# Optimization experiments

Measured on AMD Instinct MI355X. Metric: run time of the kernel, lower is better.

Reference implementation:

```python
import jax, jax.numpy as jnp
import numpy as np

N = 200_000      # nodes
E = 6_400_000    # edges (avg degree 32)
G = 2_000        # graphs
SD = 10          # state_dim
ROUNDS = 3


def setup_inputs() -> dict:
    key = jax.random.key(0)
    ks = jax.random.split(key, 10)
    node_coordinates = jax.random.normal(ks[0], (N, 3), dtype=jnp.float32)
    node_graph_index = jnp.sort(jax.random.randint(ks[1], (N,), 0, G))
    node_from = jax.random.randint(ks[2], (E,), 0, N)
    node_to = jax.random.randint(ks[3], (E,), 0, N)
    edge_lengths = jax.random.uniform(ks[4], (E, 1), dtype=jnp.float32)
    edge_vectors = jax.random.normal(ks[5], (E, 3), dtype=jnp.float32)
    # message net: Linear(14 -> 10), torch default uniform init
    lim = 1.0 / np.sqrt(SD + 4)
    W_msg = jax.random.uniform(ks[6], (SD + 4, SD), minval=-lim, maxval=lim, dtype=jnp.float32)
    b_msg = jax.random.uniform(ks[7], (SD,), minval=-lim, maxval=lim, dtype=jnp.float32)
    # output net: Linear(10 -> 4), xavier_normal weight, default bias
    W_out = jax.random.normal(ks[8], (SD, 4), dtype=jnp.float32) * np.float32(np.sqrt(2.0 / (SD + 4)))
    lim_o = 1.0 / np.sqrt(SD)
    b_out = jax.random.uniform(ks[9], (4,), minval=-lim_o, maxval=lim_o, dtype=jnp.float32)
    return dict(node_coordinates=node_coordinates, edge_lengths=edge_lengths,
                edge_vectors=edge_vectors, W_msg=W_msg, b_msg=b_msg,
                W_out=W_out, b_out=b_out, node_from=node_from, node_to=node_to,
                node_graph_index=node_graph_index, num_nodes=N, num_graphs=G)


def reference(node_coordinates, edge_lengths, edge_vectors, W_msg, b_msg,
              W_out, b_out, node_from, node_to, node_graph_index,
              num_nodes, num_graphs):
    c_from = node_coordinates[node_from]                      # (E,3) gather
    c_to = node_coordinates[node_to]                          # (E,3) gather
    coord_sum = jnp.sum(jnp.abs(c_from), axis=1, keepdims=True)       # (E,1)
    dot1 = jnp.sum(c_from * c_to, axis=1, keepdims=True)              # (E,1)
    dot2 = jnp.sum(c_from * edge_vectors, axis=1, keepdims=True)      # (E,1)
    geo = jnp.concatenate([edge_lengths, coord_sum, dot1, dot2], axis=1)  # (E,4), identical every round

    state = jnp.zeros((num_nodes, SD), dtype=node_coordinates.dtype)
    for _ in range(ROUNDS):
        inp = jnp.concatenate([state[node_from], geo], axis=1)        # (E,14)
        msg = jnp.tanh(inp @ W_msg + b_msg)                           # (E,10)
        state = state + jax.ops.segment_sum(msg, node_to, num_segments=num_nodes)

    graph_state = jax.ops.segment_sum(state, node_graph_index, num_segments=num_graphs)  # (G,10)
    ev = graph_state @ W_out + b_out                                  # (G,4)
    gamma, v, alpha, beta = jnp.split(ev, 4, axis=1)
    sp = jax.nn.softplus
    return jnp.concatenate([gamma, sp(v), sp(alpha) + 1.0, sp(beta)], axis=1)
```

## Files before the change

### kernel.cpp

```cpp
#include <hip/hip_runtime.h>
#include <hip/hip_fp16.h>
#include <math.h>

#define SD 10
#define BSZ 64
#define EB 512
#define CTHR 1024
#define BINB 10
#define NBIN_MAX 256

typedef unsigned uvec4 __attribute__((ext_vector_type(4)));
struct rec12 { unsigned x, y, z; };
union U32H2 { unsigned u; __half2 h; };

__device__ __forceinline__ float tanh_fast(float x) {
    float e = __expf(2.0f * x);
    float r = __builtin_amdgcn_rcpf(1.0f + e);
    return 1.0f - 2.0f * r;
}

__device__ __forceinline__ float softplus_f(float x) {
    return fmaxf(x, 0.0f) + log1pf(expf(-fabsf(x)));
}


__global__ __launch_bounds__(256) void coords4_kernel(
    const float* __restrict__ coords, float4* __restrict__ coords4, int N)
{
    int n = blockIdx.x * blockDim.x + threadIdx.x;
    if (n >= N) return;
    float4 c;
    c.x = coords[n * 3 + 0];
    c.y = coords[n * 3 + 1];
    c.z = coords[n * 3 + 2];
    c.w = 0.0f;
    coords4[n] = c;
}


__global__ __launch_bounds__(CTHR) void pass1_kernel(
    const float4* __restrict__ coords4,
    const float* __restrict__ elen,
    const float* __restrict__ evec,
    const int* __restrict__ nfrom,
    const int* __restrict__ nto,
    unsigned* __restrict__ s1addr,
    uvec4* __restrict__ payA,
    int E, int NBIN)
{
    __shared__ unsigned hbin[NBIN_MAX];
    __shared__ unsigned curbin[NBIN_MAX];
    int b = blockIdx.x, t = threadIdx.x;
    long long ebeg = (long long)E * b / EB;
    long long eend = (long long)E * (b + 1) / EB;

    if (t < NBIN_MAX) hbin[t] = 0;
    __syncthreads();
    for (long long e = ebeg + t; e < eend; e += CTHR)
        atomicAdd(&hbin[((unsigned)nto[e]) >> BINB], 1u);
    __syncthreads();
    {
        unsigned v = (t < NBIN_MAX) ? hbin[t] : 0u;
        for (int d = 1; d < NBIN_MAX; d <<= 1) {
            unsigned x = (t < NBIN_MAX && t >= d) ? hbin[t - d] : 0u;
            __syncthreads();
            if (t < NBIN_MAX) hbin[t] += x;
            __syncthreads();
        }
        if (t < NBIN_MAX) curbin[t] = (unsigned)ebeg + hbin[t] - v;
    }
    __syncthreads();
    if (t < NBIN) s1addr[(size_t)t * EB + b] = curbin[t];
    if (t == 0)  s1addr[(size_t)NBIN * EB + b] = (unsigned)eend;
    __syncthreads();

    long long e = ebeg + t;
    if (e < eend) {
        int nf0 = nfrom[e], nt0 = nto[e];
        float4 cf0 = coords4[nf0];
        float l0 = elen[e];
        float ex0 = evec[e*3+0], ey0 = evec[e*3+1], ez0 = evec[e*3+2];
        while (true) {
            long long e1 = e + CTHR;
            bool has1 = e1 < eend;
            int nf1 = 0, nt1 = 0; float4 cf1 = cf0;
            float l1 = 0, ex1 = 0, ey1 = 0, ez1 = 0;
            if (has1) {
                nf1 = nfrom[e1]; nt1 = nto[e1];
                cf1 = coords4[nf1];
                l1 = elen[e1]; ex1 = evec[e1*3+0]; ey1 = evec[e1*3+1]; ez1 = evec[e1*3+2];
            }
            unsigned bin = ((unsigned)nt0) >> BINB;
            unsigned pos = atomicAdd(&curbin[bin], 1u);
            float g1 = fabsf(cf0.x) + fabsf(cf0.y) + fabsf(cf0.z);
            float g3 = cf0.x * ex0 + cf0.y * ey0 + cf0.z * ez0;
            U32H2 a, c, d;
            a.h = __floats2half2_rn(l0, g1);
            c.h = __floats2half2_rn(g3, cf0.x);
            d.h = __floats2half2_rn(cf0.y, cf0.z);
            uvec4 p;
            p.x = (unsigned)nf0 | (((unsigned)nt0 & ((1u << BINB) - 1u)) << 18);
            p.y = a.u; p.z = c.u; p.w = d.u;
            payA[pos] = p;
            if (!has1) break;
            e = e1; nf0 = nf1; nt0 = nt1; cf0 = cf1;
            l0 = l1; ex0 = ex1; ey0 = ey1; ez0 = ez1;
        }
    }
}

__global__ __launch_bounds__(256) void colsum_kernel(
    const unsigned* __restrict__ s1addr, unsigned* __restrict__ binsum)
{
    __shared__ unsigned red[256];
    int q = blockIdx.x, t = threadIdx.x;
    red[t] = s1addr[(size_t)q * EB + t] + s1addr[(size_t)q * EB + t + 256];
    __syncthreads();
    for (int d = 128; d > 0; d >>= 1) {
        if (t < d) red[t] += red[t + d];
        __syncthreads();
    }
    if (t == 0) binsum[q] = red[0];
}

__global__ __launch_bounds__(256) void binstart_kernel(
    const unsigned* __restrict__ binsum, unsigned* __restrict__ binstart,
    unsigned* __restrict__ nodestart, int NBIN, int E)
{
    int t = threadIdx.x;
    unsigned b0 = binsum[0];
    for (int q = t; q <= NBIN; q += 256) binstart[q] = binsum[q] - b0;
    if (t == 0) nodestart[(size_t)NBIN << BINB] = (unsigned)E;
}

__global__ __launch_bounds__(CTHR) void pass2_kernel(
    const unsigned* __restrict__ s1addr,
    const unsigned* __restrict__ binstart,
    const float4* __restrict__ coords4,
    const uvec4* __restrict__ src,
    rec12* __restrict__ dst,
    unsigned* __restrict__ nodestart,
    int NBIN)
{
    __shared__ unsigned segst[EB];
    __shared__ unsigned spref[EB + 1];
    __shared__ unsigned hist[1 << BINB];
    __shared__ unsigned cur[1 << BINB];
    int q = blockIdx.x, t = threadIdx.x;

    if (t < EB) {
        unsigned st = s1addr[(size_t)q * EB + t];
        unsigned en = s1addr[(size_t)(q + 1) * EB + t];
        segst[t] = st;
        spref[t] = en - st;
    }
    hist[t] = 0;
    __syncthreads();
    {
        unsigned v = (t < EB) ? spref[t] : 0u;
        for (int d = 1; d < EB; d <<= 1) {
            unsigned x = (t < EB && t >= d) ? spref[t - d] : 0u;
            __syncthreads();
            if (t < EB) spref[t] += x;
            __syncthreads();
        }
        unsigned incl = (t < EB) ? spref[t] : 0u;
        __syncthreads();
        if (t < EB) spref[t] = incl - v;
        if (t == EB - 1) spref[EB] = incl;
    }
    __syncthreads();
    unsigned len = spref[EB];
    unsigned obase = binstart[q];
    const unsigned* srcw = (const unsigned*)src;

    for (unsigned i = t; i < len; i += CTHR) {
        unsigned lo = 0, hi = EB;
#pragma unroll
        for (int s = 0; s < 9; s++) {
            unsigned mid = (lo + hi) >> 1;
            if (spref[mid] <= i) lo = mid; else hi = mid;
        }
        unsigned x0 = srcw[(size_t)(segst[lo] + (i - spref[lo])) * 4];
        atomicAdd(&hist[(x0 >> 18) & ((1u << BINB) - 1u)], 1u);
    }
    __syncthreads();
    unsigned hv = hist[t];
    __syncthreads();
    for (int d = 1; d < (1 << BINB); d <<= 1) {
        unsigned x = (t >= d) ? hist[t - d] : 0u;
        __syncthreads();
        hist[t] += x;
        __syncthreads();
    }
    unsigned excl = hist[t] - hv;
    cur[t] = obase + excl;
    nodestart[((size_t)q << BINB) + t] = obase + excl;
    __syncthreads();

    for (unsigned i = t; i < len; i += CTHR) {
        unsigned lo = 0, hi = EB;
#pragma unroll
        for (int s = 0; s < 9; s++) {
            unsigned mid = (lo + hi) >> 1;
            if (spref[mid] <= i) lo = mid; else hi = mid;
        }
        uvec4 p = src[segst[lo] + (i - spref[lo])];
        unsigned key = (p.x >> 18) & ((1u << BINB) - 1u);
        unsigned pos = atomicAdd(&cur[key], 1u);
        unsigned nt = ((unsigned)q << BINB) | key;
        float4 ct = coords4[nt];
        U32H2 zc, wc;
        zc.u = p.z; wc.u = p.w;
        float g3 = __low2float(zc.h);
        float cfx = __high2float(zc.h);
        float cfy = __low2float(wc.h), cfz = __high2float(wc.h);
        float g2 = cfx * ct.x + cfy * ct.y + cfz * ct.z;
        U32H2 o; o.h = __floats2half2_rn(g2, g3);
        rec12 r;
        r.x = (p.x & 0x3FFFFu) | ((nt & (BSZ - 1u)) << 18);
        r.y = p.y;
        r.z = o.u;
        dst[pos] = r;
    }
}


__global__ __launch_bounds__(256) void wstate_kernel(
    const float* __restrict__ state, const float* __restrict__ Wm,
    const float* __restrict__ bm, __half* __restrict__ wsth, int N)
{
    int n = blockIdx.x * blockDim.x + threadIdx.x;
    if (n >= N) return;
    const float2* sp = (const float2*)(state + (size_t)n * SD);
    float s[SD];
#pragma unroll
    for (int h = 0; h < 5; h++) { float2 v = sp[h]; s[2*h] = v.x; s[2*h+1] = v.y; }
    float t[SD];
#pragma unroll
    for (int j = 0; j < SD; j++) t[j] = bm[j];
#pragma unroll
    for (int k = 0; k < SD; k++) {
#pragma unroll
        for (int j = 0; j < SD; j++) t[j] += s[k] * Wm[k * SD + j];
    }
    unsigned* dp = (unsigned*)(wsth + (size_t)n * SD);
#pragma unroll
    for (int h = 0; h < 5; h++) {
        U32H2 cv;
        cv.h = __floats2half2_rn(t[2*h], t[2*h+1]);
        dp[h] = cv.u;
    }
}

template <bool FIRST>
__global__ __launch_bounds__(256) void round_run_kernel(
    const unsigned* __restrict__ nodestart,
    const rec12* __restrict__ payload,
    const float* __restrict__ Wm,
    const float* __restrict__ bm,
    const __half* __restrict__ wsth,
    const float* __restrict__ state_prev,
    float* __restrict__ state_next,
    int N, int E)
{
    __shared__ float acc[BSZ * SD];
    int k = blockIdx.x;
    for (int i = threadIdx.x; i < BSZ * SD; i += 256) acc[i] = 0.0f;

    int lane = threadIdx.x & 63;
    int wv = threadIdx.x >> 6;
    int grp0 = lane / 10;
    bool active = grp0 < 6;
    int grp = active ? grp0 : 5;
    int j = active ? (lane - grp0 * 10) : (lane - 60);

    float w0 = Wm[10 * SD + j];
    float w1 = Wm[11 * SD + j];
    float w2 = Wm[12 * SD + j];
    float w3 = Wm[13 * SD + j];
    float bb = bm[j];
    __syncthreads();

    unsigned beg = nodestart[(size_t)k << 6];
    unsigned end = nodestart[(size_t)(k + 1) << 6];
    unsigned len = end - beg;
    unsigned Q = (len + 3) >> 2;
    unsigned rbeg = beg + (unsigned)wv * Q;
    unsigned rend = rbeg + Q; if (rend > end) rend = end;
    unsigned eclamp = (unsigned)E - 1u;

    unsigned e0 = rbeg + (unsigned)grp;
    rec12 P0 = payload[e0 <= eclamp ? e0 : eclamp];
    unsigned e1 = e0 + 6;
    rec12 P1 = payload[e1 <= eclamp ? e1 : eclamp];
    float T0 = bb, T1 = bb;
    if (!FIRST) T0 = __half2float(wsth[(size_t)(P0.x & 0x3FFFFu) * SD + j]);

    int cur_lnt = -1;
    float accv = 0.0f;

    for (unsigned base = rbeg; base < rend; base += 6) {
        unsigned e2 = base + 12 + (unsigned)grp;
        rec12 P2 = payload[e2 <= eclamp ? e2 : eclamp];
        if (!FIRST) T1 = __half2float(wsth[(size_t)(P1.x & 0x3FFFFu) * SD + j]);
        unsigned e = base + (unsigned)grp;
        if (active && e < rend) {
            int lnt = (int)((P0.x >> 18) & (BSZ - 1));
            U32H2 c01, c23;
            c01.u = P0.y; c23.u = P0.z;
            float g0 = __low2float(c01.h), g1 = __high2float(c01.h);
            float g2 = __low2float(c23.h), g3 = __high2float(c23.h);
            float t = T0 + g0 * w0 + g1 * w1 + g2 * w2 + g3 * w3;
            if (lnt != cur_lnt) {
                if (cur_lnt >= 0) atomicAdd(&acc[cur_lnt * SD + j], accv);
                accv = 0.0f;
                cur_lnt = lnt;
            }
            accv += tanh_fast(t);
        }
        P0 = P1; P1 = P2; T0 = T1;
    }
    if (active && cur_lnt >= 0) atomicAdd(&acc[cur_lnt * SD + j], accv);
    __syncthreads();

    int base_o = k * BSZ * SD;
    int lim = N * SD - base_o;
    for (int i = threadIdx.x; i < BSZ * SD; i += 256) {
        if (i < lim) {
            float v = acc[i];
            if (!FIRST) v += state_prev[base_o + i];
            state_next[base_o + i] = v;
        }
    }
}


__global__ __launch_bounds__(256) void goff_kernel(
    const int* __restrict__ gidx, unsigned* __restrict__ goff, int N, int G)
{
    int n = blockIdx.x * blockDim.x + threadIdx.x;
    if (n >= N) return;
    int g = gidx[n];
    if (n == 0) {
        for (int q = 0; q <= g; q++) goff[q] = 0;
    } else {
        int gp = gidx[n - 1];
        for (int q = gp + 1; q <= g; q++) goff[q] = (unsigned)n;
    }
    if (n == N - 1) {
        for (int q = g + 1; q <= G; q++) goff[q] = (unsigned)N;
    }
}

__global__ __launch_bounds__(256) void gsum_kernel(
    const float* __restrict__ state, const unsigned* __restrict__ goff,
    float* __restrict__ gstate, int G)
{
    int tid = blockIdx.x * blockDim.x + threadIdx.x;
    if (tid >= G * SD * 4) return;
    int s = tid & 3;
    int rest = tid >> 2;
    int g = rest / SD;
    int j = rest - g * SD;
    unsigned beg = goff[g], end = goff[g + 1];
    unsigned len = end - beg;
    unsigned b0 = beg + (len * (unsigned)s) / 4u;
    unsigned b1 = beg + (len * (unsigned)(s + 1)) / 4u;
    float a = 0.0f;
    for (unsigned n = b0; n < b1; n++) a += state[(size_t)n * SD + j];
    atomicAdd(&gstate[(size_t)g * SD + j], a);
}

__global__ __launch_bounds__(256) void out_kernel(
    const float* __restrict__ gstate, const float* __restrict__ Wo,
    const float* __restrict__ bo, float* __restrict__ out, int G)
{
    int g = blockIdx.x * blockDim.x + threadIdx.x;
    if (g >= G) return;
    float s[SD];
#pragma unroll
    for (int k = 0; k < SD; k++) s[k] = gstate[(size_t)g * SD + k];
    float ev[4];
#pragma unroll
    for (int c = 0; c < 4; c++) {
        float a = bo[c];
#pragma unroll
        for (int k = 0; k < SD; k++) a += s[k] * Wo[k * 4 + c];
        ev[c] = a;
    }
    out[g * 4 + 0] = ev[0];
    out[g * 4 + 1] = softplus_f(ev[1]);
    out[g * 4 + 2] = softplus_f(ev[2]) + 1.0f;
    out[g * 4 + 3] = softplus_f(ev[3]);
}


template <bool FIRST>
__global__ __launch_bounds__(256) void edge_kernel_fb(
    const float* __restrict__ coords, const float* __restrict__ elen,
    const float* __restrict__ evec, const float* __restrict__ Wm,
    const float* __restrict__ bm, const int* __restrict__ nfrom,
    const int* __restrict__ nto, const float* __restrict__ state_prev,
    float* __restrict__ state_next, int E)
{
    int e = blockIdx.x * blockDim.x + threadIdx.x;
    if (e >= E) return;
    int nf = nfrom[e];
    int nt = nto[e];
    float cf0 = coords[nf*3+0], cf1 = coords[nf*3+1], cf2 = coords[nf*3+2];
    float ct0 = coords[nt*3+0], ct1 = coords[nt*3+1], ct2 = coords[nt*3+2];
    float ev0 = evec[e*3+0], ev1 = evec[e*3+1], ev2 = evec[e*3+2];
    float g0 = elen[e];
    float g1 = fabsf(cf0) + fabsf(cf1) + fabsf(cf2);
    float g2 = cf0*ct0 + cf1*ct1 + cf2*ct2;
    float g3 = cf0*ev0 + cf1*ev1 + cf2*ev2;
    float acc[SD];
#pragma unroll
    for (int j = 0; j < SD; j++) {
        acc[j] = bm[j] + g0*Wm[10*SD+j] + g1*Wm[11*SD+j] + g2*Wm[12*SD+j] + g3*Wm[13*SD+j];
    }
    if (!FIRST) {
        const float2* sp = (const float2*)(state_prev + (size_t)nf * SD);
        float s[SD];
#pragma unroll
        for (int h = 0; h < 5; h++) { float2 v = sp[h]; s[2*h] = v.x; s[2*h+1] = v.y; }
#pragma unroll
        for (int k = 0; k < SD; k++) {
#pragma unroll
            for (int j = 0; j < SD; j++) acc[j] += s[k] * Wm[k*SD+j];
        }
    }
    float* dst = state_next + (size_t)nt * SD;
#pragma unroll
    for (int j = 0; j < SD; j++) atomicAdd(dst + j, tanh_fast(acc[j]));
}

__global__ __launch_bounds__(256) void graph_reduce_fb(
    const float* __restrict__ state, const int* __restrict__ gidx,
    float* __restrict__ gstate, int N)
{
    int n = blockIdx.x * blockDim.x + threadIdx.x;
    if (n >= N) return;
    int g = gidx[n];
    const float2* sp = (const float2*)(state + (size_t)n * SD);
    float* dst = gstate + (size_t)g * SD;
#pragma unroll
    for (int h = 0; h < 5; h++) {
        float2 v = sp[h];
        atomicAdd(dst + 2*h, v.x);
        atomicAdd(dst + 2*h + 1, v.y);
    }
}


extern "C" void kernel_launch(void* const* d_in, const int* in_sizes, int n_in,
                              void* d_out, int out_size, void* d_ws, size_t ws_size,
                              hipStream_t stream) {
    const float* coords = (const float*)d_in[0];
    const float* elen   = (const float*)d_in[1];
    const float* evec   = (const float*)d_in[2];
    const float* Wm     = (const float*)d_in[3];
    const float* bm     = (const float*)d_in[4];
    const float* Wo     = (const float*)d_in[5];
    const float* bo     = (const float*)d_in[6];
    const int* nfrom    = (const int*)d_in[7];
    const int* nto      = (const int*)d_in[8];
    const int* gidx     = (const int*)d_in[9];

    const int E = in_sizes[1];
    const int N = in_sizes[9];
    const int G = out_size / 4;

    const int NBIN = (N + (1 << BINB) - 1) >> BINB;
    const int NB   = (N + BSZ - 1) / BSZ;

    const int BLK = 256;
    const int ng = (N + BLK - 1) / BLK;
    const int gg = (G + BLK - 1) / BLK;

    auto align256 = [](size_t x) { return (x + 255) & ~(size_t)255; };
    const size_t state_bytes = align256((size_t)N * SD * sizeof(float));
    const size_t wst_bytes   = align256((size_t)N * SD * sizeof(__half) + 256);
    const size_t payA_bytes  = align256((size_t)E * sizeof(uvec4));
    const size_t payB_bytes  = align256((size_t)E * sizeof(rec12) + 256);
    const size_t s1a_bytes   = align256((size_t)(NBIN_MAX + 1) * EB * sizeof(unsigned));
    const size_t bsum_bytes  = align256((size_t)(NBIN_MAX + 1) * sizeof(unsigned));
    const size_t nst_bytes   = align256(((size_t)NBIN_MAX * (1 << BINB) + 2) * sizeof(unsigned));
    const size_t goff_bytes  = align256((size_t)(G + 1) * sizeof(unsigned));
    const size_t gst_bytes   = align256((size_t)G * SD * sizeof(float));
    const size_t c4_bytes    = align256((size_t)N * sizeof(float4));

    size_t o = 0;
    char* w = (char*)d_ws;
    float* stateA      = (float*)(w + o);    o += state_bytes;
    float* stateB      = (float*)(w + o);    o += state_bytes;
    __half* wsth       = (__half*)(w + o);   o += wst_bytes;
    uvec4* payA        = (uvec4*)(w + o);    o += payA_bytes;
    rec12* payB        = (rec12*)(w + o);    o += payB_bytes;
    unsigned* s1addr   = (unsigned*)(w + o); o += s1a_bytes;
    unsigned* binsum   = (unsigned*)(w + o); o += bsum_bytes;
    unsigned* binstart = (unsigned*)(w + o); o += bsum_bytes;
    unsigned* nodestart= (unsigned*)(w + o); o += nst_bytes;
    unsigned* goff     = (unsigned*)(w + o); o += goff_bytes;
    float* gstate      = (float*)(w + o);    o += gst_bytes;
    float4* coords4    = (float4*)(w + o);   o += c4_bytes;

    if (o <= ws_size && NBIN <= NBIN_MAX && N < (1 << 18)) {
        coords4_kernel<<<ng, BLK, 0, stream>>>(coords, coords4, N);
        pass1_kernel<<<EB, CTHR, 0, stream>>>(coords4, elen, evec, nfrom, nto,
                                              s1addr, payA, E, NBIN);
        colsum_kernel<<<NBIN + 1, 256, 0, stream>>>(s1addr, binsum);
        binstart_kernel<<<1, 256, 0, stream>>>(binsum, binstart, nodestart, NBIN, E);
        pass2_kernel<<<NBIN, CTHR, 0, stream>>>(s1addr, binstart, coords4,
                                                payA, payB, nodestart, NBIN);
        round_run_kernel<true><<<NB, BLK, 0, stream>>>(nodestart, payB, Wm, bm,
                                                       wsth, stateB, stateA, N, E);
        wstate_kernel<<<ng, BLK, 0, stream>>>(stateA, Wm, bm, wsth, N);
        round_run_kernel<false><<<NB, BLK, 0, stream>>>(nodestart, payB, Wm, bm,
                                                        wsth, stateA, stateB, N, E);
        wstate_kernel<<<ng, BLK, 0, stream>>>(stateB, Wm, bm, wsth, N);
        round_run_kernel<false><<<NB, BLK, 0, stream>>>(nodestart, payB, Wm, bm,
                                                        wsth, stateB, stateA, N, E);
        hipMemsetAsync(gstate, 0, (size_t)G * SD * sizeof(float), stream);
        goff_kernel<<<ng, BLK, 0, stream>>>(gidx, goff, N, G);
        gsum_kernel<<<(G * SD * 4 + BLK - 1) / BLK, BLK, 0, stream>>>(stateA, goff, gstate, G);
        out_kernel<<<gg, BLK, 0, stream>>>(gstate, Wo, bo, (float*)d_out, G);
    } else {
        const int eg = (E + BLK - 1) / BLK;
        float* gstateF = (float*)(w + 2 * state_bytes);
        hipMemsetAsync(stateA, 0, state_bytes, stream);
        hipMemsetAsync(gstateF, 0, (size_t)G * SD * sizeof(float), stream);
        edge_kernel_fb<true><<<eg, BLK, 0, stream>>>(coords, elen, evec, Wm, bm,
                                                     nfrom, nto, stateA, stateA, E);
        hipMemcpyAsync(stateB, stateA, state_bytes, hipMemcpyDeviceToDevice, stream);
        edge_kernel_fb<false><<<eg, BLK, 0, stream>>>(coords, elen, evec, Wm, bm,
                                                      nfrom, nto, stateA, stateB, E);
        hipMemcpyAsync(stateA, stateB, state_bytes, hipMemcpyDeviceToDevice, stream);
        edge_kernel_fb<false><<<eg, BLK, 0, stream>>>(coords, elen, evec, Wm, bm,
                                                      nfrom, nto, stateB, stateA, E);
        graph_reduce_fb<<<ng, BLK, 0, stream>>>(stateA, gidx, gstateF, N);
        out_kernel<<<gg, BLK, 0, stream>>>(gstateF, Wo, bo, (float*)d_out, G);
    }
}
```

Before: 726.0 us.

## Move source-coordinate gather from pass1 to pass2 and shrink payload records

The first binning pass no longer gathers source coordinates. It writes a 12-byte record holding the edge length and edge vector in half precision, down from 16 bytes, and its streaming input loads are marked nontemporal. The second pass now gathers the source coordinates (with the abs-sum precomputed in coords4.w), computes both dot products, and software-pipelines the next record and coordinate load. This cuts intermediate payload traffic and moves the random gather to a pass with better locality. The cost is an extra gather in pass2 and the edge vector stored in half precision before the dot product, which changes rounding.

```diff
diff --git a/kernel.cpp b/kernel.cpp
--- a/kernel.cpp
+++ b/kernel.cpp
@@ -33,19 +33,18 @@
     c.x = coords[n * 3 + 0];
     c.y = coords[n * 3 + 1];
     c.z = coords[n * 3 + 2];
-    c.w = 0.0f;
+    c.w = fabsf(c.x) + fabsf(c.y) + fabsf(c.z);
     coords4[n] = c;
 }
 
 
 __global__ __launch_bounds__(CTHR) void pass1_kernel(
-    const float4* __restrict__ coords4,
     const float* __restrict__ elen,
     const float* __restrict__ evec,
     const int* __restrict__ nfrom,
     const int* __restrict__ nto,
     unsigned* __restrict__ s1addr,
-    uvec4* __restrict__ payA,
+    rec12* __restrict__ payA,
     int E, int NBIN)
 {
     __shared__ unsigned hbin[NBIN_MAX];
@@ -57,7 +56,7 @@
     if (t < NBIN_MAX) hbin[t] = 0;
     __syncthreads();
     for (long long e = ebeg + t; e < eend; e += CTHR)
-        atomicAdd(&hbin[((unsigned)nto[e]) >> BINB], 1u);
+        atomicAdd(&hbin[((unsigned)__builtin_nontemporal_load(&nto[e])) >> BINB], 1u);
     __syncthreads();
     {
         unsigned v = (t < NBIN_MAX) ? hbin[t] : 0u;
@@ -74,38 +73,23 @@
     if (t == 0)  s1addr[(size_t)NBIN * EB + b] = (unsigned)eend;
     __syncthreads();
 
-    long long e = ebeg + t;
-    if (e < eend) {
-        int nf0 = nfrom[e], nt0 = nto[e];
-        float4 cf0 = coords4[nf0];
-        float l0 = elen[e];
-        float ex0 = evec[e*3+0], ey0 = evec[e*3+1], ez0 = evec[e*3+2];
-        while (true) {
-            long long e1 = e + CTHR;
-            bool has1 = e1 < eend;
-            int nf1 = 0, nt1 = 0; float4 cf1 = cf0;
-            float l1 = 0, ex1 = 0, ey1 = 0, ez1 = 0;
-            if (has1) {
-                nf1 = nfrom[e1]; nt1 = nto[e1];
-                cf1 = coords4[nf1];
-                l1 = elen[e1]; ex1 = evec[e1*3+0]; ey1 = evec[e1*3+1]; ez1 = evec[e1*3+2];
-            }
-            unsigned bin = ((unsigned)nt0) >> BINB;
-            unsigned pos = atomicAdd(&curbin[bin], 1u);
-            float g1 = fabsf(cf0.x) + fabsf(cf0.y) + fabsf(cf0.z);
-            float g3 = cf0.x * ex0 + cf0.y * ey0 + cf0.z * ez0;
-            U32H2 a, c, d;
-            a.h = __floats2half2_rn(l0, g1);
-            c.h = __floats2half2_rn(g3, cf0.x);
-            d.h = __floats2half2_rn(cf0.y, cf0.z);
-            uvec4 p;
-            p.x = (unsigned)nf0 | (((unsigned)nt0 & ((1u << BINB) - 1u)) << 18);
-            p.y = a.u; p.z = c.u; p.w = d.u;
-            payA[pos] = p;
-            if (!has1) break;
-            e = e1; nf0 = nf1; nt0 = nt1; cf0 = cf1;
-            l0 = l1; ex0 = ex1; ey0 = ey1; ez0 = ez1;
-        }
+    for (long long e = ebeg + t; e < eend; e += CTHR) {
+        int nf = __builtin_nontemporal_load(&nfrom[e]);
+        int nt = __builtin_nontemporal_load(&nto[e]);
+        float l  = __builtin_nontemporal_load(&elen[e]);
+        float ex = __builtin_nontemporal_load(&evec[e * 3 + 0]);
+        float ey = __builtin_nontemporal_load(&evec[e * 3 + 1]);
+        float ez = __builtin_nontemporal_load(&evec[e * 3 + 2]);
+        unsigned bin = ((unsigned)nt) >> BINB;
+        unsigned pos = atomicAdd(&curbin[bin], 1u);
+        U32H2 a, c;
+        a.h = __floats2half2_rn(l, ex);
+        c.h = __floats2half2_rn(ey, ez);
+        rec12 r;
+        r.x = (unsigned)nf | (((unsigned)nt & ((1u << BINB) - 1u)) << 18);
+        r.y = a.u;
+        r.z = c.u;
+        payA[pos] = r;
     }
 }
 
@@ -137,7 +121,7 @@
     const unsigned* __restrict__ s1addr,
     const unsigned* __restrict__ binstart,
     const float4* __restrict__ coords4,
-    const uvec4* __restrict__ src,
+    const rec12* __restrict__ src,
     rec12* __restrict__ dst,
     unsigned* __restrict__ nodestart,
     int NBIN)
@@ -181,7 +165,7 @@
             unsigned mid = (lo + hi) >> 1;
             if (spref[mid] <= i) lo = mid; else hi = mid;
         }
-        unsigned x0 = srcw[(size_t)(segst[lo] + (i - spref[lo])) * 4];
+        unsigned x0 = srcw[(size_t)(segst[lo] + (i - spref[lo])) * 3];
         atomicAdd(&hist[(x0 >> 18) & ((1u << BINB) - 1u)], 1u);
     }
     __syncthreads();
@@ -198,30 +182,52 @@
     nodestart[((size_t)q << BINB) + t] = obase + excl;
     __syncthreads();
 
+    rec12 p0; float4 cf0;
+    {
+        unsigned i0 = t;
+        if (i0 < len) {
+            unsigned lo = 0, hi = EB;
+#pragma unroll
+            for (int s = 0; s < 9; s++) {
+                unsigned mid = (lo + hi) >> 1;
+                if (spref[mid] <= i0) lo = mid; else hi = mid;
+            }
+            p0 = src[segst[lo] + (i0 - spref[lo])];
+            cf0 = coords4[p0.x & 0x3FFFFu];
+        }
+    }
     for (unsigned i = t; i < len; i += CTHR) {
-        unsigned lo = 0, hi = EB;
-#pragma unroll
-        for (int s = 0; s < 9; s++) {
-            unsigned mid = (lo + hi) >> 1;
-            if (spref[mid] <= i) lo = mid; else hi = mid;
-        }
-        uvec4 p = src[segst[lo] + (i - spref[lo])];
-        unsigned key = (p.x >> 18) & ((1u << BINB) - 1u);
+        unsigned i1 = i + CTHR;
+        rec12 p1 = p0; float4 cf1 = cf0;
+        if (i1 < len) {
+            unsigned lo = 0, hi = EB;
+#pragma unroll
+            for (int s = 0; s < 9; s++) {
+                unsigned mid = (lo + hi) >> 1;
+                if (spref[mid] <= i1) lo = mid; else hi = mid;
+            }
+            p1 = src[segst[lo] + (i1 - spref[lo])];
+            cf1 = coords4[p1.x & 0x3FFFFu];
+        }
+        unsigned key = (p0.x >> 18) & ((1u << BINB) - 1u);
         unsigned pos = atomicAdd(&cur[key], 1u);
         unsigned nt = ((unsigned)q << BINB) | key;
         float4 ct = coords4[nt];
-        U32H2 zc, wc;
-        zc.u = p.z; wc.u = p.w;
-        float g3 = __low2float(zc.h);
-        float cfx = __high2float(zc.h);
-        float cfy = __low2float(wc.h), cfz = __high2float(wc.h);
-        float g2 = cfx * ct.x + cfy * ct.y + cfz * ct.z;
-        U32H2 o; o.h = __floats2half2_rn(g2, g3);
+        U32H2 ya, za;
+        ya.u = p0.y; za.u = p0.z;
+        float g0 = __low2float(ya.h), ev0 = __high2float(ya.h);
+        float ev1 = __low2float(za.h), ev2 = __high2float(za.h);
+        float g2 = cf0.x * ct.x + cf0.y * ct.y + cf0.z * ct.z;
+        float g3 = cf0.x * ev0 + cf0.y * ev1 + cf0.z * ev2;
+        U32H2 oy, oz;
+        oy.h = __floats2half2_rn(g0, cf0.w);
+        oz.h = __floats2half2_rn(g2, g3);
         rec12 r;
-        r.x = (p.x & 0x3FFFFu) | ((nt & (BSZ - 1u)) << 18);
-        r.y = p.y;
-        r.z = o.u;
+        r.x = (p0.x & 0x3FFFFu) | ((nt & (BSZ - 1u)) << 18);
+        r.y = oy.u;
+        r.z = oz.u;
         dst[pos] = r;
+        p0 = p1; cf0 = cf1;
     }
 }
 
@@ -482,7 +488,7 @@
     auto align256 = [](size_t x) { return (x + 255) & ~(size_t)255; };
     const size_t state_bytes = align256((size_t)N * SD * sizeof(float));
     const size_t wst_bytes   = align256((size_t)N * SD * sizeof(__half) + 256);
-    const size_t payA_bytes  = align256((size_t)E * sizeof(uvec4));
+    const size_t payA_bytes  = align256((size_t)E * sizeof(rec12) + 256);
     const size_t payB_bytes  = align256((size_t)E * sizeof(rec12) + 256);
     const size_t s1a_bytes   = align256((size_t)(NBIN_MAX + 1) * EB * sizeof(unsigned));
     const size_t bsum_bytes  = align256((size_t)(NBIN_MAX + 1) * sizeof(unsigned));
@@ -496,7 +502,7 @@
     float* stateA      = (float*)(w + o);    o += state_bytes;
     float* stateB      = (float*)(w + o);    o += state_bytes;
     __half* wsth       = (__half*)(w + o);   o += wst_bytes;
-    uvec4* payA        = (uvec4*)(w + o);    o += payA_bytes;
+    rec12* payA        = (rec12*)(w + o);    o += payA_bytes;
     rec12* payB        = (rec12*)(w + o);    o += payB_bytes;
     unsigned* s1addr   = (unsigned*)(w + o); o += s1a_bytes;
     unsigned* binsum   = (unsigned*)(w + o); o += bsum_bytes;
@@ -508,7 +514,7 @@
 
     if (o <= ws_size && NBIN <= NBIN_MAX && N < (1 << 18)) {
         coords4_kernel<<<ng, BLK, 0, stream>>>(coords, coords4, N);
-        pass1_kernel<<<EB, CTHR, 0, stream>>>(coords4, elen, evec, nfrom, nto,
+        pass1_kernel<<<EB, CTHR, 0, stream>>>(elen, evec, nfrom, nto,
                                               s1addr, payA, E, NBIN);
         colsum_kernel<<<NBIN + 1, 256, 0, stream>>>(s1addr, binsum);
         binstart_kernel<<<1, 256, 0, stream>>>(binsum, binstart, nodestart, NBIN, E);
```

New measurement: 702.3 us. 1.03x faster.
